# Kernel optimization log

Hardware: AMD Instinct MI355X
Metric: run time of the kernel (lower is better)

## Reference

```python
import jax, jax.numpy as jnp
import numpy as np

BN_EPS = 1e-5


def setup_inputs() -> dict:
    key = jax.random.key(0)
    k1, k2, k3, k4 = jax.random.split(key, 4)
    B, C_in, T, V = 64, 64, 300, 25
    K, C_out = 3, 64
    x = jax.random.normal(k1, (B, C_in, T, V), dtype=jnp.float32)
    # 1x1 Conv2d weight collapsed to (K*C_out, C_in); bias (K*C_out,)
    W = jax.random.normal(k2, (K * C_out, C_in), dtype=jnp.float32) * (1.0 / np.sqrt(C_in))
    b = jax.random.normal(k3, (K * C_out,), dtype=jnp.float32) * 0.02
    A = jax.random.uniform(k4, (K, V, V), dtype=jnp.float32)
    gamma = jnp.ones((C_out,), dtype=jnp.float32)
    beta = jnp.zeros((C_out,), dtype=jnp.float32)
    return {"x": x, "W": W, "b": b, "A": A, "gamma": gamma, "beta": beta}


def reference(x, W, b, A, gamma, beta):
    B, C_in, T, V = x.shape
    K = A.shape[0]
    C_out = W.shape[0] // K
    # 1x1 conv == per-pixel matmul over channels
    x_conv = jnp.einsum('bctv,oc->botv', x, W) + b[None, :, None, None]
    # split into K partitions: (B, K, C_out, T, V)
    x_conv = x_conv.reshape(B, K, C_out, T, V)
    # fused per-partition graph matmul + sum over partitions
    out = jnp.einsum('bkctv,kvw->bctw', x_conv, A)
    # BatchNorm2d (training mode: batch statistics over B, T, V)
    mean = jnp.mean(out, axis=(0, 2, 3), keepdims=True)
    var = jnp.var(out, axis=(0, 2, 3), keepdims=True)  # biased variance
    out_hat = (out - mean) * jax.lax.rsqrt(var + BN_EPS)
    return out_hat * gamma[None, :, None, None] + beta[None, :, None, None]
```

## Files before the change

### kernel.cpp

```cpp
#include <hip/hip_runtime.h>
#include <stdint.h>


#define TT 4
#define NPIX (TT * 25)
#define NT1 7
#define NBLK 4800

typedef short bf16x8 __attribute__((ext_vector_type(8)));
typedef float f32x4 __attribute__((ext_vector_type(4)));

__device__ inline short f2bf(float f) {
    union { float f; uint32_t u; } v; v.f = f;
    uint32_t u = v.u;
    u += 0x7fffu + ((u >> 16) & 1u);
    return (short)(u >> 16);
}

__global__ __launch_bounds__(256, 2) void sgc_main(
    const float* __restrict__ x, const float* __restrict__ W,
    const float* __restrict__ bias, const float* __restrict__ A,
    float* __restrict__ out, float* __restrict__ stats_part)
{
    __shared__ __align__(16) short xT[7168];
    __shared__ __align__(16) short Ylds[24576];
    __shared__ __align__(16) short Acat[3072];

    const int tid  = threadIdx.x;
    const int lane = tid & 63;
    const int wave = tid >> 6;
    const int bid  = blockIdx.x;
    const int b    = bid / 75;
    const int t0   = (bid % 75) * TT;

    bf16x8 z8 = {0,0,0,0,0,0,0,0};
    #pragma unroll
    for (int j = 0; j < 12; ++j)
        *(bf16x8*)&Ylds[(tid + 256 * j) * 8] = z8;

    {
        const size_t xbase = (size_t)b * 480000 + (size_t)t0 * 25;
        #pragma unroll
        for (int j = 0; j < 7; ++j) {
            int e4 = tid + 256 * j;
            if (e4 < 1600) {
                int ci = e4 / 25;
                int n  = (e4 % 25) * 4;
                const float4 v = *(const float4*)&x[xbase + (size_t)ci * 7500 + n];
                #pragma unroll
                for (int i = 0; i < 4; ++i) {
                    int nn = n + i;
                    int sidx = ((nn >> 4) * 2 + (ci >> 5)) * 512
                             + ((ci >> 3) & 3) * 128 + (nn & 15) * 8 + (ci & 7);
                    xT[sidx] = f2bf(((const float*)&v)[i]);
                }
            }
        }
    }

    #pragma unroll
    for (int j = 0; j < 12; ++j) {
        int s    = tid + 256 * j;
        int tile = s >> 9;
        int q    = s & 511;
        int oct  = q >> 7;
        int wl   = (q >> 3) & 15;
        int jj   = s & 7;
        int nt2  = tile / 3, kb2 = tile % 3;
        int w    = nt2 * 16 + wl;
        int kv   = kb2 * 32 + oct * 8 + jj;
        int k    = kv >> 5, v = kv & 31;
        float val = (v < 25 && w < 25) ? A[(k * 25 + v) * 25 + w] : 0.f;
        Acat[s] = f2bf(val);
    }

    bf16x8 wfrag[3][2];
    #pragma unroll
    for (int mti = 0; mti < 3; ++mti) {
        int o = (wave * 3 + mti) * 16 + (lane & 15);
        #pragma unroll
        for (int kb = 0; kb < 2; ++kb) {
            int ci0 = kb * 32 + (lane >> 4) * 8;
            const float4 f0 = *(const float4*)&W[o * 64 + ci0];
            const float4 f1 = *(const float4*)&W[o * 64 + ci0 + 4];
            bf16x8 f;
            f[0] = f2bf(f0.x); f[1] = f2bf(f0.y); f[2] = f2bf(f0.z); f[3] = f2bf(f0.w);
            f[4] = f2bf(f1.x); f[5] = f2bf(f1.y); f[6] = f2bf(f1.z); f[7] = f2bf(f1.w);
            wfrag[mti][kb] = f;
        }
    }

    float bval[3][4];
    #pragma unroll
    for (int mti = 0; mti < 3; ++mti)
        #pragma unroll
        for (int r = 0; r < 4; ++r)
            bval[mti][r] = bias[(wave * 3 + mti) * 16 + (lane >> 4) * 4 + r];

    __syncthreads();

    f32x4 acc[3][NT1];
    #pragma unroll
    for (int mti = 0; mti < 3; ++mti)
        #pragma unroll
        for (int nt = 0; nt < NT1; ++nt) {
            f32x4 zf = {0.f, 0.f, 0.f, 0.f};
            acc[mti][nt] = zf;
        }

    #pragma unroll
    for (int nt = 0; nt < NT1; ++nt) {
        bf16x8 xb0 = *(const bf16x8*)&xT[((nt * 2 + 0) * 64 + lane) * 8];
        bf16x8 xb1 = *(const bf16x8*)&xT[((nt * 2 + 1) * 64 + lane) * 8];
        #pragma unroll
        for (int mti = 0; mti < 3; ++mti) {
            acc[mti][nt] = __builtin_amdgcn_mfma_f32_16x16x32_bf16(
                wfrag[mti][0], xb0, acc[mti][nt], 0, 0, 0);
            acc[mti][nt] = __builtin_amdgcn_mfma_f32_16x16x32_bf16(
                wfrag[mti][1], xb1, acc[mti][nt], 0, 0, 0);
        }
    }

    #pragma unroll
    for (int nt = 0; nt < NT1; ++nt) {
        int n = nt * 16 + (lane & 15);
        if (n < NPIX) {
            int t = n / 25, v = n % 25;
            #pragma unroll
            for (int mti = 0; mti < 3; ++mti) {
                int obase = (wave * 3 + mti) * 16 + (lane >> 4) * 4;
                #pragma unroll
                for (int r = 0; r < 4; ++r) {
                    int o = obase + r;
                    int k = o >> 6, c = o & 63;
                    int kv = k * 32 + v;
                    float val = acc[mti][nt][r] + bval[mti][r];
                    int sidx = ((t * 4 + (c >> 4)) * 3 + k) * 512
                             + ((kv >> 3) & 3) * 128 + (c & 15) * 8 + (kv & 7);
                    Ylds[sidx] = f2bf(val);
                }
            }
        }
    }
    __syncthreads();

    bf16x8 bfrag2[2][3];
    #pragma unroll
    for (int nt2 = 0; nt2 < 2; ++nt2)
        #pragma unroll
        for (int kb2 = 0; kb2 < 3; ++kb2)
            bfrag2[nt2][kb2] = *(const bf16x8*)&Acat[((nt2 * 3 + kb2) * 64 + lane) * 8];

    float ssum[4] = {0.f, 0.f, 0.f, 0.f};
    float ssq[4]  = {0.f, 0.f, 0.f, 0.f};
    const int c0 = wave * 16 + (lane >> 4) * 4;

    #pragma unroll
    for (int t = 0; t < TT; ++t) {
        bf16x8 a2[3];
        #pragma unroll
        for (int kb2 = 0; kb2 < 3; ++kb2)
            a2[kb2] = *(const bf16x8*)&Ylds[(((t * 4 + wave) * 3 + kb2) * 64 + lane) * 8];

        f32x4 acc2[2];
        #pragma unroll
        for (int nt2 = 0; nt2 < 2; ++nt2) {
            f32x4 zf = {0.f, 0.f, 0.f, 0.f};
            acc2[nt2] = zf;
            #pragma unroll
            for (int kb2 = 0; kb2 < 3; ++kb2)
                acc2[nt2] = __builtin_amdgcn_mfma_f32_16x16x32_bf16(
                    a2[kb2], bfrag2[nt2][kb2], acc2[nt2], 0, 0, 0);
        }

        #pragma unroll
        for (int nt2 = 0; nt2 < 2; ++nt2) {
            int w = nt2 * 16 + (lane & 15);
            bool valid = (w < 25);
            #pragma unroll
            for (int r = 0; r < 4; ++r) {
                float val = acc2[nt2][r];
                if (valid) {
                    out[(size_t)((b * 64 + c0 + r) * 300 + t0 + t) * 25 + w] = val;
                    ssum[r] += val;
                    ssq[r]  += val * val;
                }
            }
        }
    }

    #pragma unroll
    for (int r = 0; r < 4; ++r) {
        float s = ssum[r], q = ssq[r];
        #pragma unroll
        for (int d = 1; d < 16; d <<= 1) {
            s += __shfl_xor(s, d);
            q += __shfl_xor(q, d);
        }
        if ((lane & 15) == 0) {
            int c = c0 + r;
            int slot = bid & 63;
            atomicAdd(&stats_part[slot * 128 + c], s);
            atomicAdd(&stats_part[slot * 128 + 64 + c], q);
        }
    }
}

__global__ void sgc_finalize(const float* __restrict__ stats_part,
                             const float* __restrict__ gamma,
                             const float* __restrict__ beta,
                             float* __restrict__ scaleshift)
{
    int c = threadIdx.x;
    float s = 0.f, q = 0.f;
    #pragma unroll 8
    for (int slot = 0; slot < 64; ++slot) {
        s += stats_part[slot * 128 + c];
        q += stats_part[slot * 128 + 64 + c];
    }
    const float invN = 1.f / 480000.f;
    float mean = s * invN;
    float var  = q * invN - mean * mean;
    float rstd = rsqrtf(var + 1e-5f);
    float sc = rstd * gamma[c];
    scaleshift[c]      = sc;
    scaleshift[64 + c] = beta[c] - mean * sc;
}

__global__ __launch_bounds__(256) void sgc_norm(float* __restrict__ out,
                                                const float* __restrict__ scaleshift)
{
    const int total4 = 30720000 / 4;
    int stride = gridDim.x * 256;
    for (int i = blockIdx.x * 256 + threadIdx.x; i < total4; i += stride) {
        int c = (i / 1875) & 63;
        float sc = scaleshift[c], sh = scaleshift[64 + c];
        float4 v = *((float4*)out + i);
        v.x = v.x * sc + sh;
        v.y = v.y * sc + sh;
        v.z = v.z * sc + sh;
        v.w = v.w * sc + sh;
        *((float4*)out + i) = v;
    }
}

extern "C" void kernel_launch(void* const* d_in, const int* in_sizes, int n_in,
                              void* d_out, int out_size, void* d_ws, size_t ws_size,
                              hipStream_t stream)
{
    const float* x     = (const float*)d_in[0];
    const float* W     = (const float*)d_in[1];
    const float* bias  = (const float*)d_in[2];
    const float* A     = (const float*)d_in[3];
    const float* gamma = (const float*)d_in[4];
    const float* beta  = (const float*)d_in[5];
    float* out = (float*)d_out;

    float* stats      = (float*)d_ws;
    float* scaleshift = stats + 64 * 128;

    hipMemsetAsync(stats, 0, 64 * 128 * sizeof(float), stream);
    sgc_main<<<NBLK, 256, 0, stream>>>(x, W, bias, A, out, stats);
    sgc_finalize<<<1, 64, 0, stream>>>(stats, gamma, beta, scaleshift);
    sgc_norm<<<4096, 256, 0, stream>>>(out, scaleshift);
}
```

Measured before the change: 347.2 us.

## Load x fragments directly from global, shrink time tile, pack bf16 conversions

The first GEMM now builds its B-operand fragments straight from global memory in registers and no longer stages x through an LDS transpose buffer. This removes one LDS round-trip and a barrier. The time tile drops from 4 to 3 frames (6400 blocks), which shrinks LDS use and allows 3 blocks per CU. bf16 conversion switches to the packed v_cvt_pk_bf16_f32 instruction, and only the padding region of Ylds is zero-filled. The direct x loads are strided scalar loads that may coalesce worse, and the smaller tile adds per-block overhead.

Measured after the change: 354.7 us. +2.2%, slower.

```diff
diff --git a/kernel.cpp b/kernel.cpp
--- a/kernel.cpp
+++ b/kernel.cpp
@@ -2,13 +2,15 @@
 #include <stdint.h>
 
 
-#define TT 4
+#define TT 3
 #define NPIX (TT * 25)
-#define NT1 7
-#define NBLK 4800
+#define NT1 5
+#define NBLK 6400
 
 typedef short bf16x8 __attribute__((ext_vector_type(8)));
 typedef float f32x4 __attribute__((ext_vector_type(4)));
+
+union frag_u { bf16x8 v; uint32_t u[4]; };
 
 __device__ inline short f2bf(float f) {
     union { float f; uint32_t u; } v; v.f = f;
@@ -17,88 +19,78 @@
     return (short)(u >> 16);
 }
 
-__global__ __launch_bounds__(256, 2) void sgc_main(
+__device__ inline uint32_t cvtpk(float lo, float hi) {
+    uint32_t d;
+    asm("v_cvt_pk_bf16_f32 %0, %1, %2" : "=v"(d) : "v"(lo), "v"(hi));
+    return d;
+}
+
+__global__ __launch_bounds__(256, 3) void sgc_main(
     const float* __restrict__ x, const float* __restrict__ W,
     const float* __restrict__ bias, const float* __restrict__ A,
     float* __restrict__ out, float* __restrict__ stats_part)
 {
-    __shared__ __align__(16) short xT[7168];
-    __shared__ __align__(16) short Ylds[24576];
+    __shared__ __align__(16) short Ylds[18432];
     __shared__ __align__(16) short Acat[3072];
 
     const int tid  = threadIdx.x;
     const int lane = tid & 63;
     const int wave = tid >> 6;
+    const int q4   = lane >> 4;
+    const int wl   = lane & 15;
     const int bid  = blockIdx.x;
-    const int b    = bid / 75;
-    const int t0   = (bid % 75) * TT;
-
-    bf16x8 z8 = {0,0,0,0,0,0,0,0};
-    #pragma unroll
-    for (int j = 0; j < 12; ++j)
-        *(bf16x8*)&Ylds[(tid + 256 * j) * 8] = z8;
+    const int b    = bid / 100;
+    const int t0   = (bid % 100) * TT;
 
     {
-        const size_t xbase = (size_t)b * 480000 + (size_t)t0 * 25;
-        #pragma unroll
-        for (int j = 0; j < 7; ++j) {
-            int e4 = tid + 256 * j;
-            if (e4 < 1600) {
-                int ci = e4 / 25;
-                int n  = (e4 % 25) * 4;
-                const float4 v = *(const float4*)&x[xbase + (size_t)ci * 7500 + n];
-                #pragma unroll
-                for (int i = 0; i < 4; ++i) {
-                    int nn = n + i;
-                    int sidx = ((nn >> 4) * 2 + (ci >> 5)) * 512
-                             + ((ci >> 3) & 3) * 128 + (nn & 15) * 8 + (ci & 7);
-                    xT[sidx] = f2bf(((const float*)&v)[i]);
-                }
+        bf16x8 z8 = {0,0,0,0,0,0,0,0};
+        #pragma unroll
+        for (int j = 0; j < 3; ++j) {
+            int s = tid + 256 * j;
+            if (s < 576)
+                *(bf16x8*)&Ylds[(s >> 4) * 512 + 384 + (s & 15) * 8] = z8;
+        }
+    }
+
+    #pragma unroll
+    for (int j = 0; j < 2; ++j) {
+        int g = tid + 256 * j;
+        if (g < 384) {
+            int tile = g >> 6;
+            int kb2  = tile >> 1, nt2 = tile & 1;
+            int oct  = (g >> 4) & 3;
+            int w    = nt2 * 16 + (g & 15);
+            frag_u fr;
+            #pragma unroll
+            for (int p = 0; p < 4; ++p) {
+                int v0 = oct * 8 + 2 * p;
+                float a0 = (w < 25 && v0     < 25) ? A[(kb2 * 25 + v0) * 25 + w]     : 0.f;
+                float a1 = (w < 25 && v0 + 1 < 25) ? A[(kb2 * 25 + v0 + 1) * 25 + w] : 0.f;
+                fr.u[p] = cvtpk(a0, a1);
             }
-        }
-    }
-
-    #pragma unroll
-    for (int j = 0; j < 12; ++j) {
-        int s    = tid + 256 * j;
-        int tile = s >> 9;
-        int q    = s & 511;
-        int oct  = q >> 7;
-        int wl   = (q >> 3) & 15;
-        int jj   = s & 7;
-        int nt2  = tile / 3, kb2 = tile % 3;
-        int w    = nt2 * 16 + wl;
-        int kv   = kb2 * 32 + oct * 8 + jj;
-        int k    = kv >> 5, v = kv & 31;
-        float val = (v < 25 && w < 25) ? A[(k * 25 + v) * 25 + w] : 0.f;
-        Acat[s] = f2bf(val);
+            *(bf16x8*)&Acat[g * 8] = fr.v;
+        }
     }
 
     bf16x8 wfrag[3][2];
     #pragma unroll
     for (int mti = 0; mti < 3; ++mti) {
-        int o = (wave * 3 + mti) * 16 + (lane & 15);
+        int o = (wave * 3 + mti) * 16 + wl;
         #pragma unroll
         for (int kb = 0; kb < 2; ++kb) {
-            int ci0 = kb * 32 + (lane >> 4) * 8;
+            int ci0 = kb * 32 + q4 * 8;
             const float4 f0 = *(const float4*)&W[o * 64 + ci0];
             const float4 f1 = *(const float4*)&W[o * 64 + ci0 + 4];
-            bf16x8 f;
-            f[0] = f2bf(f0.x); f[1] = f2bf(f0.y); f[2] = f2bf(f0.z); f[3] = f2bf(f0.w);
-            f[4] = f2bf(f1.x); f[5] = f2bf(f1.y); f[6] = f2bf(f1.z); f[7] = f2bf(f1.w);
-            wfrag[mti][kb] = f;
-        }
-    }
-
-    float bval[3][4];
-    #pragma unroll
-    for (int mti = 0; mti < 3; ++mti)
-        #pragma unroll
-        for (int r = 0; r < 4; ++r)
-            bval[mti][r] = bias[(wave * 3 + mti) * 16 + (lane >> 4) * 4 + r];
-
-    __syncthreads();
-
+            frag_u fr;
+            fr.u[0] = cvtpk(f0.x, f0.y);
+            fr.u[1] = cvtpk(f0.z, f0.w);
+            fr.u[2] = cvtpk(f1.x, f1.y);
+            fr.u[3] = cvtpk(f1.z, f1.w);
+            wfrag[mti][kb] = fr.v;
+        }
+    }
+
+    const float* xp = x + (size_t)b * 480000 + (size_t)t0 * 25;
     f32x4 acc[3][NT1];
     #pragma unroll
     for (int mti = 0; mti < 3; ++mti)
@@ -110,35 +102,54 @@
 
     #pragma unroll
     for (int nt = 0; nt < NT1; ++nt) {
-        bf16x8 xb0 = *(const bf16x8*)&xT[((nt * 2 + 0) * 64 + lane) * 8];
-        bf16x8 xb1 = *(const bf16x8*)&xT[((nt * 2 + 1) * 64 + lane) * 8];
+        int n = nt * 16 + wl;
+        if (n > NPIX - 1) n = NPIX - 1;
+        int loff = q4 * 60000 + n;
+        bf16x8 xb[2];
+        #pragma unroll
+        for (int kb = 0; kb < 2; ++kb) {
+            float xv[8];
+            #pragma unroll
+            for (int jj = 0; jj < 8; ++jj)
+                xv[jj] = (xp + (kb * 32 + jj) * 7500)[loff];
+            frag_u fr;
+            #pragma unroll
+            for (int p = 0; p < 4; ++p)
+                fr.u[p] = cvtpk(xv[2 * p], xv[2 * p + 1]);
+            xb[kb] = fr.v;
+        }
         #pragma unroll
         for (int mti = 0; mti < 3; ++mti) {
             acc[mti][nt] = __builtin_amdgcn_mfma_f32_16x16x32_bf16(
-                wfrag[mti][0], xb0, acc[mti][nt], 0, 0, 0);
+                wfrag[mti][0], xb[0], acc[mti][nt], 0, 0, 0);
             acc[mti][nt] = __builtin_amdgcn_mfma_f32_16x16x32_bf16(
-                wfrag[mti][1], xb1, acc[mti][nt], 0, 0, 0);
-        }
-    }
+                wfrag[mti][1], xb[1], acc[mti][nt], 0, 0, 0);
+        }
+    }
+
+    float4 bv[3];
+    #pragma unroll
+    for (int mti = 0; mti < 3; ++mti)
+        bv[mti] = *(const float4*)&bias[(wave * 3 + mti) * 16 + q4 * 4];
+
+    __syncthreads();
 
     #pragma unroll
     for (int nt = 0; nt < NT1; ++nt) {
-        int n = nt * 16 + (lane & 15);
+        int n = nt * 16 + wl;
         if (n < NPIX) {
             int t = n / 25, v = n % 25;
             #pragma unroll
             for (int mti = 0; mti < 3; ++mti) {
-                int obase = (wave * 3 + mti) * 16 + (lane >> 4) * 4;
+                int wt = wave * 3 + mti;
+                int k  = wt >> 2, cq = wt & 3;
+                int kv = k * 32 + v;
+                int sbase = ((t * 4 + cq) * 3 + k) * 512
+                          + ((kv >> 3) & 3) * 128 + q4 * 32 + (kv & 7);
+                const float* bp = (const float*)&bv[mti];
                 #pragma unroll
-                for (int r = 0; r < 4; ++r) {
-                    int o = obase + r;
-                    int k = o >> 6, c = o & 63;
-                    int kv = k * 32 + v;
-                    float val = acc[mti][nt][r] + bval[mti][r];
-                    int sidx = ((t * 4 + (c >> 4)) * 3 + k) * 512
-                             + ((kv >> 3) & 3) * 128 + (c & 15) * 8 + (kv & 7);
-                    Ylds[sidx] = f2bf(val);
-                }
+                for (int r = 0; r < 4; ++r)
+                    Ylds[sbase + r * 8] = f2bf(acc[mti][nt][r] + bp[r]);
             }
         }
     }
@@ -149,11 +160,11 @@
     for (int nt2 = 0; nt2 < 2; ++nt2)
         #pragma unroll
         for (int kb2 = 0; kb2 < 3; ++kb2)
-            bfrag2[nt2][kb2] = *(const bf16x8*)&Acat[((nt2 * 3 + kb2) * 64 + lane) * 8];
+            bfrag2[nt2][kb2] = *(const bf16x8*)&Acat[((kb2 * 2 + nt2) * 64 + lane) * 8];
 
     float ssum[4] = {0.f, 0.f, 0.f, 0.f};
     float ssq[4]  = {0.f, 0.f, 0.f, 0.f};
-    const int c0 = wave * 16 + (lane >> 4) * 4;
+    const int c0 = wave * 16 + q4 * 4;
 
     #pragma unroll
     for (int t = 0; t < TT; ++t) {
@@ -175,7 +186,7 @@
 
         #pragma unroll
         for (int nt2 = 0; nt2 < 2; ++nt2) {
-            int w = nt2 * 16 + (lane & 15);
+            int w = nt2 * 16 + wl;
             bool valid = (w < 25);
             #pragma unroll
             for (int r = 0; r < 4; ++r) {
@@ -197,7 +208,7 @@
             s += __shfl_xor(s, d);
             q += __shfl_xor(q, d);
         }
-        if ((lane & 15) == 0) {
+        if (wl == 0) {
             int c = c0 + r;
             int slot = bid & 63;
             atomicAdd(&stats_part[slot * 128 + c], s);
```
